# Performance work log

Hardware: AMD Instinct MI355X
Metric: run time of the kernel (lower is better)

The kernel has to match this reference:

```python
import jax, jax.numpy as jnp
import numpy as np

N, D, K = 500000, 128, 2048

def setup_inputs() -> dict:
    key = jax.random.key(0)
    kx, kp = jax.random.split(key)
    x = jax.random.normal(kx, (N, D), dtype=jnp.float32)
    p = jax.random.normal(kp, (D,), dtype=jnp.float32)
    return {"x": x, "p": p, "k": K}

def reference(x, p, k):
    # y = x @ p / ||p||  -> [N]
    y = (x @ p) / jnp.linalg.norm(p)
    top_vals, top_idx = jax.lax.top_k(y, k)          # [k], [k]
    # gather top-k rows and scale by tanh of their scores
    out = x[top_idx] * jnp.tanh(top_vals)[:, None]   # [k, D]
    return out
```

## Files before the change

kernel.cpp:

```cpp
#include <hip/hip_runtime.h>
#include <hip/hip_bf16.h>


#define HIST_BITS 12
#define HIST_BINS (1 << HIST_BITS)
#define HIST_SHIFT (32 - HIST_BITS)
#define SORTN 8192
#define SLICES 8

__device__ __forceinline__ unsigned mono_key(float f) {
    unsigned u = __float_as_uint(f);
    return (u & 0x80000000u) ? ~u : (u | 0x80000000u);
}
__device__ __forceinline__ float mono_key_inv(unsigned mk) {
    unsigned u = (mk & 0x80000000u) ? (mk ^ 0x80000000u) : ~mk;
    return __uint_as_float(u);
}

__global__ void score_kernel(const float* __restrict__ x, const float* __restrict__ p,
                             float* __restrict__ y, int N, int rpw) {
    int lane = threadIdx.x & 63;
    int half = lane >> 5;
    int l32  = lane & 31;
    long long gwave = ((long long)blockIdx.x * blockDim.x + threadIdx.x) >> 6;
    long long start = gwave * rpw;
    if (start >= N) return;

    float4 pq = ((const float4*)p)[l32];
    double pp = (double)pq.x * pq.x + (double)pq.y * pq.y +
                (double)pq.z * pq.z + (double)pq.w * pq.w;
    #pragma unroll
    for (int off = 16; off > 0; off >>= 1) pp += __shfl_xor(pp, off, 64);
    double rinv = 1.0 / sqrt(pp);

    long long rend = start + rpw; if (rend > N) rend = N;
    for (long long r0 = start; r0 < rend; r0 += 4) {
        long long rowA = r0 + half;
        long long rowB = r0 + 2 + half;
        bool vb = (r0 + 2) < rend;
        float4 xa = ((const float4*)(x + rowA * 128))[l32];
        float4 xb = vb ? ((const float4*)(x + rowB * 128))[l32]
                       : make_float4(0.f, 0.f, 0.f, 0.f);
        double dA = (double)xa.x * pq.x + (double)xa.y * pq.y +
                    (double)xa.z * pq.z + (double)xa.w * pq.w;
        double dB = (double)xb.x * pq.x + (double)xb.y * pq.y +
                    (double)xb.z * pq.z + (double)xb.w * pq.w;
        #pragma unroll
        for (int off = 16; off > 0; off >>= 1) {
            dA += __shfl_xor(dA, off, 64);
            dB += __shfl_xor(dB, off, 64);
        }
        if (l32 == 0) {
            y[rowA] = (float)(dA * rinv);
            if (vb) y[rowB] = (float)(dB * rinv);
        }
    }
}

__global__ void hist_kernel(const float* __restrict__ y, unsigned* __restrict__ hist, int N) {
    __shared__ unsigned h[4][HIST_BINS];
    for (int i = threadIdx.x; i < 4 * HIST_BINS; i += blockDim.x) h[0][i] = 0;
    __syncthreads();
    int sub = (threadIdx.x >> 6) & 3;
    int stride = gridDim.x * blockDim.x;
    for (int i = blockIdx.x * blockDim.x + threadIdx.x; i < N; i += stride)
        atomicAdd(&h[sub][mono_key(y[i]) >> HIST_SHIFT], 1u);
    __syncthreads();
    for (int i = threadIdx.x; i < HIST_BINS; i += blockDim.x) {
        unsigned v = h[0][i] + h[1][i] + h[2][i] + h[3][i];
        if (v) atomicAdd(&hist[i], v);
    }
}

__global__ void threshold_kernel(const unsigned* __restrict__ hist,
                                 const int* __restrict__ kptr, int* __restrict__ res) {
    __shared__ unsigned s[HIST_BINS];
    int t = threadIdx.x;
    for (int i = t; i < HIST_BINS; i += 1024) s[i] = hist[i];
    __syncthreads();
    for (int off = 1; off < HIST_BINS; off <<= 1) {
        unsigned v[HIST_BINS / 1024];
        #pragma unroll
        for (int j = 0; j < HIST_BINS / 1024; j++) {
            int i = t + j * 1024;
            v[j] = s[i] + ((i + off < HIST_BINS) ? s[i + off] : 0u);
        }
        __syncthreads();
        #pragma unroll
        for (int j = 0; j < HIST_BINS / 1024; j++) s[t + j * 1024] = v[j];
        __syncthreads();
    }
    int k = *kptr;
    #pragma unroll
    for (int j = 0; j < HIST_BINS / 1024; j++) {
        int i = t + j * 1024;
        int c     = (int)s[i];
        int cnext = (i + 1 < HIST_BINS) ? (int)s[i + 1] : 0;
        if (c >= k && cnext < k) { res[0] = i; res[1] = cnext; }
    }
}

__global__ void compact_kernel(const float* __restrict__ y, const int* __restrict__ res,
                               unsigned long long* __restrict__ pairs, int* __restrict__ cnt,
                               int N) {
    __shared__ int lcnt, lbase;
    if (threadIdx.x == 0) lcnt = 0;
    __syncthreads();
    int B = res[0];
    int i = blockIdx.x * blockDim.x + threadIdx.x;
    int lpos = -1;
    unsigned mk = 0;
    if (i < N) {
        mk = mono_key(y[i]);
        if ((int)(mk >> HIST_SHIFT) >= B) lpos = atomicAdd(&lcnt, 1);
    }
    __syncthreads();
    if (threadIdx.x == 0 && lcnt > 0) lbase = atomicAdd(cnt, lcnt);
    __syncthreads();
    if (lpos >= 0) {
        int pos = lbase + lpos;
        if (pos < SORTN)
            pairs[pos] = ((unsigned long long)mk << 32) | (unsigned)~(unsigned)i;
    }
}

__global__ void rank_count_kernel(const unsigned long long* __restrict__ pairs,
                                  const int* __restrict__ cnt,
                                  int* __restrict__ rankpart) {
    __shared__ unsigned long long s[SORTN / SLICES];
    int n = *cnt; if (n > SORTN) n = SORTN;
    if ((int)(blockIdx.x * blockDim.x) >= n) return;
    int npad = (n + 4 * SLICES - 1) & ~(4 * SLICES - 1);
    int slen = npad / SLICES;
    int sbeg = blockIdx.y * slen;
    for (int i = threadIdx.x; i < slen; i += blockDim.x) {
        int gi = sbeg + i;
        s[i] = (gi < n) ? pairs[gi] : 0ull;
    }
    __syncthreads();
    int c = blockIdx.x * blockDim.x + threadIdx.x;
    if (c >= n) return;
    unsigned long long my = pairs[c];
    int r = 0;
    for (int i = 0; i < slen; i += 4)
        r += (int)(s[i] > my) + (int)(s[i+1] > my) + (int)(s[i+2] > my) + (int)(s[i+3] > my);
    rankpart[blockIdx.y * SORTN + c] = r;
}

__global__ void rank_scatter_kernel(const unsigned long long* __restrict__ pairs,
                                    const int* __restrict__ cnt,
                                    const int* __restrict__ rankpart,
                                    unsigned long long* __restrict__ spairs, int K) {
    int n = *cnt; if (n > SORTN) n = SORTN;
    int c = blockIdx.x * blockDim.x + threadIdx.x;
    if (c >= n) return;
    int r = 0;
    #pragma unroll
    for (int sl = 0; sl < SLICES; sl++) r += rankpart[sl * SORTN + c];
    if (r < K) spairs[r] = pairs[c];
}

__global__ void gather_kernel(const float* __restrict__ x,
                              const unsigned long long* __restrict__ spairs,
                              float* __restrict__ out) {
    int j = blockIdx.x;
    unsigned long long key = spairs[j];
    unsigned mk  = (unsigned)(key >> 32);
    unsigned idx = ~(unsigned)(key & 0xFFFFFFFFull);
    float scale = tanhf(mono_key_inv(mk));
    int t = threadIdx.x;
    out[(size_t)j * 128 + t] = x[(size_t)idx * 128 + t] * scale;
}

extern "C" void kernel_launch(void* const* d_in, const int* in_sizes, int n_in,
                              void* d_out, int out_size, void* d_ws, size_t ws_size,
                              hipStream_t stream) {
    const float* x = (const float*)d_in[0];
    const float* p = (const float*)d_in[1];
    const int*   kptr = (const int*)d_in[2];
    float* out = (float*)d_out;

    const int D = in_sizes[1];
    const int N = in_sizes[0] / D;
    const int K = out_size / D;
    (void)n_in; (void)ws_size;

    unsigned char* w = (unsigned char*)d_ws;
    float* y = (float*)w;
    size_t off = ((size_t)N * sizeof(float) + 255) & ~(size_t)255;
    unsigned* hist = (unsigned*)(w + off);
    int* cnt = (int*)(w + off + HIST_BINS * sizeof(unsigned));
    int* res = cnt + 1;
    size_t off2 = (off + HIST_BINS * sizeof(unsigned) + 3 * sizeof(int) + 255) & ~(size_t)255;
    unsigned long long* pairs = (unsigned long long*)(w + off2);
    unsigned long long* spairs = pairs + SORTN;
    int* rankpart = (int*)(spairs + SORTN);

    hipMemsetAsync(hist, 0, HIST_BINS * sizeof(unsigned) + sizeof(int), stream);

    {
        const int blocks = 2048;
        long long total_waves = (long long)blocks * 256 / 64;
        int rpw = (int)((N + total_waves - 1) / total_waves);
        rpw = (rpw + 1) & ~1;
        score_kernel<<<blocks, 256, 0, stream>>>(x, p, y, N, rpw);
    }
    hist_kernel<<<64, 1024, 0, stream>>>(y, hist, N);
    threshold_kernel<<<1, 1024, 0, stream>>>(hist, kptr, res);
    compact_kernel<<<(N + 255) / 256, 256, 0, stream>>>(y, res, pairs, cnt, N);
    rank_count_kernel<<<dim3(SORTN / 256, SLICES), 256, 0, stream>>>(pairs, cnt, rankpart);
    rank_scatter_kernel<<<SORTN / 256, 256, 0, stream>>>(pairs, cnt, rankpart, spairs, K);
    gather_kernel<<<K, 128, 0, stream>>>(x, spairs, out);
}
```

Before: 396.6 us.

## Fuse threshold and rank-scatter via last-block tickets, fold memset, vectorize passes

Removes the memset by zeroing the workspace inside the score kernel. The threshold scan moves into the last-finishing histogram block, and the rank scatter into the last-finishing rank block, using atomic tickets. Histogram, compaction and gather are vectorized with float4 loads. This cuts kernel launches and small-kernel tail latency, at the cost of fence and atomic ordering complexity and a serial tail in a single block.

```diff
diff --git a/kernel.cpp b/kernel.cpp
--- a/kernel.cpp
+++ b/kernel.cpp
@@ -1,5 +1,4 @@
 #include <hip/hip_runtime.h>
-#include <hip/hip_bf16.h>
 
 
 #define HIST_BITS 12
@@ -8,6 +7,8 @@
 #define SORTN 8192
 #define SLICES 8
 
+#define ZWORDS (HIST_BINS + 1 + 2 + 2 + SORTN)
+
 __device__ __forceinline__ unsigned mono_key(float f) {
     unsigned u = __float_as_uint(f);
     return (u & 0x80000000u) ? ~u : (u | 0x80000000u);
@@ -18,7 +19,17 @@
 }
 
 __global__ void score_kernel(const float* __restrict__ x, const float* __restrict__ p,
-                             float* __restrict__ y, int N, int rpw) {
+                             float* __restrict__ y, int N, int rpw,
+                             unsigned* __restrict__ zbase) {
+    if (blockIdx.x < 64) {
+        const int zpb = (ZWORDS + 63) >> 6;
+        int base = blockIdx.x * zpb;
+        for (int i = threadIdx.x; i < zpb; i += 256) {
+            int wi = base + i;
+            if (wi < ZWORDS) zbase[wi] = 0u;
+        }
+    }
+
     int lane = threadIdx.x & 63;
     int half = lane >> 5;
     int l32  = lane & 31;
@@ -57,46 +68,62 @@
     }
 }
 
-__global__ void hist_kernel(const float* __restrict__ y, unsigned* __restrict__ hist, int N) {
+__global__ void hist_kernel(const float* __restrict__ y, unsigned* __restrict__ hist,
+                            int* __restrict__ res, const int* __restrict__ kptr,
+                            unsigned* __restrict__ ticket, int N) {
     __shared__ unsigned h[4][HIST_BINS];
     for (int i = threadIdx.x; i < 4 * HIST_BINS; i += blockDim.x) h[0][i] = 0;
     __syncthreads();
     int sub = (threadIdx.x >> 6) & 3;
     int stride = gridDim.x * blockDim.x;
-    for (int i = blockIdx.x * blockDim.x + threadIdx.x; i < N; i += stride)
+    int N4 = N >> 2;
+    const float4* y4 = (const float4*)y;
+    for (int i = blockIdx.x * blockDim.x + threadIdx.x; i < N4; i += stride) {
+        float4 v = y4[i];
+        atomicAdd(&h[sub][mono_key(v.x) >> HIST_SHIFT], 1u);
+        atomicAdd(&h[sub][mono_key(v.y) >> HIST_SHIFT], 1u);
+        atomicAdd(&h[sub][mono_key(v.z) >> HIST_SHIFT], 1u);
+        atomicAdd(&h[sub][mono_key(v.w) >> HIST_SHIFT], 1u);
+    }
+    for (int i = (N & ~3) + blockIdx.x * blockDim.x + threadIdx.x; i < N; i += stride)
         atomicAdd(&h[sub][mono_key(y[i]) >> HIST_SHIFT], 1u);
     __syncthreads();
     for (int i = threadIdx.x; i < HIST_BINS; i += blockDim.x) {
         unsigned v = h[0][i] + h[1][i] + h[2][i] + h[3][i];
         if (v) atomicAdd(&hist[i], v);
     }
-}
-
-__global__ void threshold_kernel(const unsigned* __restrict__ hist,
-                                 const int* __restrict__ kptr, int* __restrict__ res) {
-    __shared__ unsigned s[HIST_BINS];
-    int t = threadIdx.x;
-    for (int i = t; i < HIST_BINS; i += 1024) s[i] = hist[i];
+    __syncthreads();
+    __threadfence();
+    __shared__ int lastf;
+    if (threadIdx.x == 0)
+        lastf = (atomicAdd(ticket, 1u) == (unsigned)(gridDim.x - 1));
+    __syncthreads();
+    if (!lastf) return;
+
+    __threadfence();
+    unsigned* s = h[0];
+    for (int i = threadIdx.x; i < HIST_BINS; i += blockDim.x)
+        s[i] = __hip_atomic_load(&hist[i], __ATOMIC_RELAXED, __HIP_MEMORY_SCOPE_AGENT);
     __syncthreads();
     for (int off = 1; off < HIST_BINS; off <<= 1) {
         unsigned v[HIST_BINS / 1024];
         #pragma unroll
         for (int j = 0; j < HIST_BINS / 1024; j++) {
-            int i = t + j * 1024;
+            int i = threadIdx.x + j * 1024;
             v[j] = s[i] + ((i + off < HIST_BINS) ? s[i + off] : 0u);
         }
         __syncthreads();
         #pragma unroll
-        for (int j = 0; j < HIST_BINS / 1024; j++) s[t + j * 1024] = v[j];
+        for (int j = 0; j < HIST_BINS / 1024; j++) s[threadIdx.x + j * 1024] = v[j];
         __syncthreads();
     }
     int k = *kptr;
     #pragma unroll
     for (int j = 0; j < HIST_BINS / 1024; j++) {
-        int i = t + j * 1024;
+        int i = threadIdx.x + j * 1024;
         int c     = (int)s[i];
         int cnext = (i + 1 < HIST_BINS) ? (int)s[i + 1] : 0;
-        if (c >= k && cnext < k) { res[0] = i; res[1] = cnext; }
+        if (c >= k && cnext < k) res[0] = i;
     }
 }
 
@@ -107,69 +134,99 @@
     if (threadIdx.x == 0) lcnt = 0;
     __syncthreads();
     int B = res[0];
+    int N4 = N >> 2;
     int i = blockIdx.x * blockDim.x + threadIdx.x;
-    int lpos = -1;
-    unsigned mk = 0;
-    if (i < N) {
-        mk = mono_key(y[i]);
-        if ((int)(mk >> HIST_SHIFT) >= B) lpos = atomicAdd(&lcnt, 1);
-    }
+    unsigned mk[4];
+    int okmask = 0, nloc = 0;
+    int base = i * 4;
+    if (i < N4) {
+        float4 v = ((const float4*)y)[i];
+        mk[0] = mono_key(v.x); mk[1] = mono_key(v.y);
+        mk[2] = mono_key(v.z); mk[3] = mono_key(v.w);
+        #pragma unroll
+        for (int j = 0; j < 4; j++)
+            if ((int)(mk[j] >> HIST_SHIFT) >= B) { okmask |= 1 << j; nloc++; }
+    } else {
+        #pragma unroll
+        for (int j = 0; j < 4; j++) {
+            int idx = base + j;
+            if (idx < N) {
+                mk[j] = mono_key(y[idx]);
+                if ((int)(mk[j] >> HIST_SHIFT) >= B) { okmask |= 1 << j; nloc++; }
+            }
+        }
+    }
+    int lpos = 0;
+    if (nloc) lpos = atomicAdd(&lcnt, nloc);
     __syncthreads();
     if (threadIdx.x == 0 && lcnt > 0) lbase = atomicAdd(cnt, lcnt);
     __syncthreads();
-    if (lpos >= 0) {
+    if (nloc) {
         int pos = lbase + lpos;
-        if (pos < SORTN)
-            pairs[pos] = ((unsigned long long)mk << 32) | (unsigned)~(unsigned)i;
-    }
-}
-
-__global__ void rank_count_kernel(const unsigned long long* __restrict__ pairs,
-                                  const int* __restrict__ cnt,
-                                  int* __restrict__ rankpart) {
+        #pragma unroll
+        for (int j = 0; j < 4; j++) {
+            if (okmask & (1 << j)) {
+                if (pos < SORTN)
+                    pairs[pos] = ((unsigned long long)mk[j] << 32) | (unsigned)~(unsigned)(base + j);
+                pos++;
+            }
+        }
+    }
+}
+
+__global__ void rank_kernel(const unsigned long long* __restrict__ pairs,
+                            const int* __restrict__ cnt,
+                            int* __restrict__ rank,
+                            unsigned long long* __restrict__ spairs, int K,
+                            unsigned* __restrict__ ticket) {
     __shared__ unsigned long long s[SORTN / SLICES];
     int n = *cnt; if (n > SORTN) n = SORTN;
-    if ((int)(blockIdx.x * blockDim.x) >= n) return;
-    int npad = (n + 4 * SLICES - 1) & ~(4 * SLICES - 1);
-    int slen = npad / SLICES;
-    int sbeg = blockIdx.y * slen;
-    for (int i = threadIdx.x; i < slen; i += blockDim.x) {
-        int gi = sbeg + i;
-        s[i] = (gi < n) ? pairs[gi] : 0ull;
-    }
-    __syncthreads();
-    int c = blockIdx.x * blockDim.x + threadIdx.x;
-    if (c >= n) return;
-    unsigned long long my = pairs[c];
-    int r = 0;
-    for (int i = 0; i < slen; i += 4)
-        r += (int)(s[i] > my) + (int)(s[i+1] > my) + (int)(s[i+2] > my) + (int)(s[i+3] > my);
-    rankpart[blockIdx.y * SORTN + c] = r;
-}
-
-__global__ void rank_scatter_kernel(const unsigned long long* __restrict__ pairs,
-                                    const int* __restrict__ cnt,
-                                    const int* __restrict__ rankpart,
-                                    unsigned long long* __restrict__ spairs, int K) {
-    int n = *cnt; if (n > SORTN) n = SORTN;
-    int c = blockIdx.x * blockDim.x + threadIdx.x;
-    if (c >= n) return;
-    int r = 0;
-    #pragma unroll
-    for (int sl = 0; sl < SLICES; sl++) r += rankpart[sl * SORTN + c];
-    if (r < K) spairs[r] = pairs[c];
+    bool active = ((int)(blockIdx.x * blockDim.x) < n);
+    if (active) {
+        int npad = (n + 4 * SLICES - 1) & ~(4 * SLICES - 1);
+        int slen = npad / SLICES;
+        int sbeg = blockIdx.y * slen;
+        for (int i = threadIdx.x; i < slen; i += blockDim.x) {
+            int gi = sbeg + i;
+            s[i] = (gi < n) ? pairs[gi] : 0ull;
+        }
+        __syncthreads();
+        int c = blockIdx.x * blockDim.x + threadIdx.x;
+        if (c < n) {
+            unsigned long long my = pairs[c];
+            int r = 0;
+            for (int i = 0; i < slen; i += 4)
+                r += (int)(s[i] > my) + (int)(s[i+1] > my) + (int)(s[i+2] > my) + (int)(s[i+3] > my);
+            if (r) atomicAdd(&rank[c], r);
+        }
+    }
+    __syncthreads();
+    __threadfence();
+    __shared__ int lastf;
+    if (threadIdx.x == 0)
+        lastf = (atomicAdd(ticket, 1u) == (unsigned)(gridDim.x * gridDim.y - 1));
+    __syncthreads();
+    if (!lastf) return;
+
+    __threadfence();
+    for (int c = threadIdx.x; c < n; c += blockDim.x) {
+        int r = __hip_atomic_load(&rank[c], __ATOMIC_RELAXED, __HIP_MEMORY_SCOPE_AGENT);
+        if (r < K) spairs[r] = pairs[c];
+    }
 }
 
 __global__ void gather_kernel(const float* __restrict__ x,
                               const unsigned long long* __restrict__ spairs,
-                              float* __restrict__ out) {
-    int j = blockIdx.x;
+                              float* __restrict__ out, int K) {
+    int t = blockIdx.x * blockDim.x + threadIdx.x;
+    int j = t >> 5, lane = t & 31;
+    if (j >= K) return;
     unsigned long long key = spairs[j];
-    unsigned mk  = (unsigned)(key >> 32);
+    float scale = tanhf(mono_key_inv((unsigned)(key >> 32)));
     unsigned idx = ~(unsigned)(key & 0xFFFFFFFFull);
-    float scale = tanhf(mono_key_inv(mk));
-    int t = threadIdx.x;
-    out[(size_t)j * 128 + t] = x[(size_t)idx * 128 + t] * scale;
+    float4 v = ((const float4*)(x + (size_t)idx * 128))[lane];
+    ((float4*)(out + (size_t)j * 128))[lane] =
+        make_float4(v.x * scale, v.y * scale, v.z * scale, v.w * scale);
 }
 
 extern "C" void kernel_launch(void* const* d_in, const int* in_sizes, int n_in,
@@ -187,28 +244,29 @@
 
     unsigned char* w = (unsigned char*)d_ws;
     float* y = (float*)w;
-    size_t off = ((size_t)N * sizeof(float) + 255) & ~(size_t)255;
-    unsigned* hist = (unsigned*)(w + off);
-    int* cnt = (int*)(w + off + HIST_BINS * sizeof(unsigned));
+    size_t off1 = ((size_t)N * sizeof(float) + 255) & ~(size_t)255;
+    unsigned* zbase = (unsigned*)(w + off1);
+    unsigned* hist = zbase;
+    int* cnt = (int*)(zbase + HIST_BINS);
     int* res = cnt + 1;
-    size_t off2 = (off + HIST_BINS * sizeof(unsigned) + 3 * sizeof(int) + 255) & ~(size_t)255;
+    unsigned* tickets = (unsigned*)(res + 2);
+    int* rank = (int*)(tickets + 2);
+    size_t off2 = (off1 + (size_t)ZWORDS * 4 + 255) & ~(size_t)255;
     unsigned long long* pairs = (unsigned long long*)(w + off2);
     unsigned long long* spairs = pairs + SORTN;
-    int* rankpart = (int*)(spairs + SORTN);
-
-    hipMemsetAsync(hist, 0, HIST_BINS * sizeof(unsigned) + sizeof(int), stream);
 
     {
         const int blocks = 2048;
         long long total_waves = (long long)blocks * 256 / 64;
         int rpw = (int)((N + total_waves - 1) / total_waves);
         rpw = (rpw + 1) & ~1;
-        score_kernel<<<blocks, 256, 0, stream>>>(x, p, y, N, rpw);
-    }
-    hist_kernel<<<64, 1024, 0, stream>>>(y, hist, N);
-    threshold_kernel<<<1, 1024, 0, stream>>>(hist, kptr, res);
-    compact_kernel<<<(N + 255) / 256, 256, 0, stream>>>(y, res, pairs, cnt, N);
-    rank_count_kernel<<<dim3(SORTN / 256, SLICES), 256, 0, stream>>>(pairs, cnt, rankpart);
-    rank_scatter_kernel<<<SORTN / 256, 256, 0, stream>>>(pairs, cnt, rankpart, spairs, K);
-    gather_kernel<<<K, 128, 0, stream>>>(x, spairs, out);
-}
+        score_kernel<<<blocks, 256, 0, stream>>>(x, p, y, N, rpw, zbase);
+    }
+    hist_kernel<<<64, 1024, 0, stream>>>(y, hist, res, kptr, &tickets[0], N);
+    {
+        int blocks = (((N + 3) / 4) + 255) / 256;
+        compact_kernel<<<blocks, 256, 0, stream>>>(y, res, pairs, cnt, N);
+    }
+    rank_kernel<<<dim3(SORTN / 256, SLICES), 256, 0, stream>>>(pairs, cnt, rank, spairs, K, &tickets[1]);
+    gather_kernel<<<(K * 32 + 255) / 256, 256, 0, stream>>>(x, spairs, out, K);
+}
```

After: 408.7 us. 3.0% more time.
